# Performance work log

Measured on AMD Instinct MI355X. Metric: run time of the kernel, lower is better.

## Reference

```python
import jax, jax.numpy as jnp
import numpy as np

VOCAB, EMBED, SEQ, UNITS, BATCH = 10000, 100, 80, 64, 16384


def setup_inputs() -> dict:
    key = jax.random.key(0)
    ks = jax.random.split(key, 8)
    s = 0.05
    return {
        "tokens": jax.random.randint(ks[0], (BATCH, SEQ), 0, VOCAB, dtype=jnp.int32),
        "emb": jax.random.normal(ks[1], (VOCAB, EMBED), jnp.float32) * s,
        "Wx1": jax.random.normal(ks[2], (EMBED, UNITS), jnp.float32) * s,
        "Wh1": jax.random.normal(ks[3], (UNITS, UNITS), jnp.float32) * s,
        "b1": jnp.zeros((UNITS,), jnp.float32),
        "Wx2": jax.random.normal(ks[4], (UNITS, UNITS), jnp.float32) * s,
        "Wh2": jax.random.normal(ks[5], (UNITS, UNITS), jnp.float32) * s,
        "b2": jnp.zeros((UNITS,), jnp.float32),
        "Wd": jax.random.normal(ks[6], (UNITS, 1), jnp.float32) * s,
        "bd": jnp.zeros((1,), jnp.float32),
    }


def _simple_rnn(x, Wx, Wh, b):
    """SimpleRNN (eval mode): h_t = tanh(x_t @ Wx + h_{t-1} @ Wh + b).
    x: (B, T, E) -> all hidden states (B, T, U)."""
    # precompute input projection once (big GEMM), scan only does the small recurrent matmul
    xp = jnp.einsum("bte,eu->btu", x, Wx) + b  # (B, T, U)

    def step(h, xt):
        h = jnp.tanh(xt + h @ Wh)
        return h, h

    h0 = jnp.zeros((x.shape[0], Wh.shape[0]), x.dtype)
    _, hs = jax.lax.scan(step, h0, jnp.swapaxes(xp, 0, 1))  # (T, B, U)
    return jnp.swapaxes(hs, 0, 1)  # (B, T, U)


def reference(tokens, emb, Wx1, Wh1, b1, Wx2, Wh2, b2, Wd, bd):
    x = emb[tokens]                              # (B, T, E) embedding lookup
    h1 = _simple_rnn(x, Wx1, Wh1, b1)            # (B, T, U) return_sequences=True
    h2 = _simple_rnn(h1, Wx2, Wh2, b2)[:, -1]    # (B, U)    last state only
    return jax.nn.sigmoid(h2 @ Wd + bd)          # (B, 1)
```

## Files before the change

### kernel.cpp

```cpp
#include <hip/hip_runtime.h>
#include <hip/hip_bf16.h>


#define BATCH 16384
#define SEQ   80
#define EMBED 100
#define UNITS 64
#define ROWS  16
#define VOCAB 10000

typedef __attribute__((ext_vector_type(8))) _Float16 f16x8;
typedef __attribute__((ext_vector_type(4))) float f32x4;
typedef __attribute__((ext_vector_type(2))) float f32x2;
typedef __attribute__((ext_vector_type(4))) int   i32x4;
typedef __attribute__((ext_vector_type(2))) int   i32x2;

using h2 = decltype(__builtin_amdgcn_cvt_pkrtz(0.f, 0.f));

static __device__ __forceinline__ f32x2 tanh2(f32x2 x) {
    f32x2 u = x * x;
    f32x2 w = x * u;
    f32x2 p = u * 0.13333333f + (-0.33333333f);
    return w * p + x;
}

static __device__ __forceinline__ f16x8 ash(i32x4 v) {
    return __builtin_bit_cast(f16x8, v);
}

__global__ __launch_bounds__(256) void xp_prep(const float* __restrict__ emb,
                                               const float* __restrict__ Wx1,
                                               const float* __restrict__ b1,
                                               float* __restrict__ xp) {
    const int v = blockIdx.x * 4 + (threadIdx.x >> 6);
    const int u = threadIdx.x & 63;
    const float* er = emb + (size_t)v * EMBED;
    const float* wc = Wx1 + u;
    float acc = b1[u];
#pragma unroll 5
    for (int k4 = 0; k4 < EMBED / 4; ++k4) {
        f32x4 e = *reinterpret_cast<const f32x4*>(er + k4 * 4);
        acc += e[0] * wc[(k4 * 4 + 0) * UNITS];
        acc += e[1] * wc[(k4 * 4 + 1) * UNITS];
        acc += e[2] * wc[(k4 * 4 + 2) * UNITS];
        acc += e[3] * wc[(k4 * 4 + 3) * UNITS];
    }
    xp[(size_t)v * UNITS + u] = acc;
}

__global__ __launch_bounds__(64)
void rnn_fused(const int* __restrict__ tokens,
               const float* __restrict__ xpT,
               const float* __restrict__ Wh1,
               const float* __restrict__ Wx2,
               const float* __restrict__ Wh2,
               const float* __restrict__ b2,
               const float* __restrict__ Wd,
               const float* __restrict__ bd,
               float* __restrict__ out)
{
    __shared__ int tokL[ROWS][SEQ + 1];

    const int lane = threadIdx.x;
    const int c    = lane & 15;
    const int q    = lane >> 4;
    const int rowBase = blockIdx.x * ROWS;

    for (int i = lane; i < ROWS * SEQ; i += 64) {
        int r = i / SEQ, tt = i - r * SEQ;
        tokL[r][tt] = tokens[rowBase * SEQ + i];
    }
    __syncthreads();

    auto loadW = [&](const float* W, f16x8 (&dst)[2][4]) {
#pragma unroll
        for (int kt = 0; kt < 2; ++kt)
#pragma unroll
            for (int mt = 0; mt < 4; ++mt) {
                f16x8 v;
#pragma unroll
                for (int j = 0; j < 8; ++j) {
                    int u = kt * 32 + ((j >> 2) << 4) + q * 4 + (j & 3);
                    v[j] = (_Float16)W[u * UNITS + mt * 16 + c];
                }
                dst[kt][mt] = v;
            }
    };

    f16x8 awh1[2][4], awx2[2][4], awh2[2][4];
    loadW(Wh1, awh1);
    loadW(Wx2, awx2);
    loadW(Wh2, awh2);

    f32x4 b2C[4];
#pragma unroll
    for (int mt = 0; mt < 4; ++mt)
#pragma unroll
        for (int r = 0; r < 4; ++r)
            b2C[mt][r] = b2[mt * 16 + q * 4 + r];

    const h2 kC1h = __builtin_amdgcn_cvt_pkrtz( 0.13333333f,  0.13333333f);
    const h2 kC0h = __builtin_amdgcn_cvt_pkrtz(-0.33333333f, -0.33333333f);

    auto tanh_pack4 = [&](f32x4 v) -> i32x2 {
        h2 lo = __builtin_amdgcn_cvt_pkrtz(v[0], v[1]);
        h2 hi = __builtin_amdgcn_cvt_pkrtz(v[2], v[3]);
        h2 ulo = lo * lo,        uhi = hi * hi;
        h2 wlo = ulo * lo,       whi = uhi * hi;
        h2 plo = ulo * kC1h + kC0h, phi = uhi * kC1h + kC0h;
        h2 rlo = wlo * plo + lo, rhi = whi * phi + hi;
        i32x2 r;
        r[0] = __builtin_bit_cast(int, rlo);
        r[1] = __builtin_bit_cast(int, rhi);
        return r;
    };

    const int* tokC = &tokL[c][0];

    auto gatherXP = [&](int tk, f32x4 (&dst)[4]) {
        const float* p = xpT + (unsigned)tk * UNITS + q * 4;
        dst[0] = *reinterpret_cast<const f32x4*>(p);
        dst[1] = *reinterpret_cast<const f32x4*>(p + 16);
        dst[2] = *reinterpret_cast<const f32x4*>(p + 32);
        dst[3] = *reinterpret_cast<const f32x4*>(p + 48);
    };

    i32x4 h1[2] = {(i32x4){0,0,0,0}, (i32x4){0,0,0,0}};
    i32x4 h2s[2] = {(i32x4){0,0,0,0}, (i32x4){0,0,0,0}};
    f32x4 xp0[4], xp1[4];
    gatherXP(tokC[0], xp0);
    gatherXP(tokC[1], xp1);

    auto tanhP = [&](f32x4 (&a)[4], i32x4 (&h)[2]) {
        i32x2 p0 = tanh_pack4(a[0]), p1 = tanh_pack4(a[1]);
        i32x2 p2 = tanh_pack4(a[2]), p3 = tanh_pack4(a[3]);
        h[0] = (i32x4){p0[0], p0[1], p1[0], p1[1]};
        h[1] = (i32x4){p2[0], p2[1], p3[0], p3[1]};
    };

    auto body = [&](f32x4 (&xpS)[4], bool doPre, int tp) {
        f32x4 aL1[4], aL2[4];
#pragma unroll
        for (int mt = 0; mt < 4; ++mt)
            aL1[mt] = __builtin_amdgcn_mfma_f32_16x16x32_f16(awh1[0][mt], ash(h1[0]), xpS[mt], 0, 0, 0);
#pragma unroll
        for (int mt = 0; mt < 4; ++mt)
            aL2[mt] = __builtin_amdgcn_mfma_f32_16x16x32_f16(awx2[0][mt], ash(h1[0]), b2C[mt], 0, 0, 0);
#pragma unroll
        for (int mt = 0; mt < 4; ++mt)
            aL1[mt] = __builtin_amdgcn_mfma_f32_16x16x32_f16(awh1[1][mt], ash(h1[1]), aL1[mt], 0, 0, 0);
#pragma unroll
        for (int mt = 0; mt < 4; ++mt)
            aL2[mt] = __builtin_amdgcn_mfma_f32_16x16x32_f16(awx2[1][mt], ash(h1[1]), aL2[mt], 0, 0, 0);
#pragma unroll
        for (int mt = 0; mt < 4; ++mt)
            aL2[mt] = __builtin_amdgcn_mfma_f32_16x16x32_f16(awh2[0][mt], ash(h2s[0]), aL2[mt], 0, 0, 0);
#pragma unroll
        for (int mt = 0; mt < 4; ++mt)
            aL2[mt] = __builtin_amdgcn_mfma_f32_16x16x32_f16(awh2[1][mt], ash(h2s[1]), aL2[mt], 0, 0, 0);
        if (doPre) gatherXP(tp, xpS);
        tanhP(aL1, h1);
        tanhP(aL2, h2s);
    };

    {
        f32x4 aL1[4];
#pragma unroll
        for (int mt = 0; mt < 4; ++mt)
            aL1[mt] = __builtin_amdgcn_mfma_f32_16x16x32_f16(awh1[0][mt], ash(h1[0]), xp0[mt], 0, 0, 0);
#pragma unroll
        for (int mt = 0; mt < 4; ++mt)
            aL1[mt] = __builtin_amdgcn_mfma_f32_16x16x32_f16(awh1[1][mt], ash(h1[1]), aL1[mt], 0, 0, 0);
        gatherXP(tokC[2], xp0);
        tanhP(aL1, h1);
    }

#pragma unroll 1
    for (int tt = 1; tt <= 75; tt += 2) {
        body(xp1, true, tokC[tt + 2]);
        body(xp0, true, tokC[tt + 3]);
    }
    body(xp1, true, tokC[79]);
    body(xp0, false, 0);
    body(xp1, false, 0);

    {
        f32x4 a[4];
#pragma unroll
        for (int mt = 0; mt < 4; ++mt)
            a[mt] = __builtin_amdgcn_mfma_f32_16x16x32_f16(awx2[0][mt], ash(h1[0]), b2C[mt], 0, 0, 0);
#pragma unroll
        for (int mt = 0; mt < 4; ++mt)
            a[mt] = __builtin_amdgcn_mfma_f32_16x16x32_f16(awx2[1][mt], ash(h1[1]), a[mt], 0, 0, 0);
#pragma unroll
        for (int mt = 0; mt < 4; ++mt)
            a[mt] = __builtin_amdgcn_mfma_f32_16x16x32_f16(awh2[0][mt], ash(h2s[0]), a[mt], 0, 0, 0);
#pragma unroll
        for (int mt = 0; mt < 4; ++mt)
            a[mt] = __builtin_amdgcn_mfma_f32_16x16x32_f16(awh2[1][mt], ash(h2s[1]), a[mt], 0, 0, 0);

        f32x4 wdC[4];
#pragma unroll
        for (int mt = 0; mt < 4; ++mt)
#pragma unroll
            for (int r = 0; r < 4; ++r)
                wdC[mt][r] = Wd[mt * 16 + q * 4 + r];
        const float bdv = bd[0];

        float p = 0.f;
#pragma unroll
        for (int mt = 0; mt < 4; ++mt) {
            f32x2 lo = tanh2((f32x2){a[mt][0], a[mt][1]});
            f32x2 hi = tanh2((f32x2){a[mt][2], a[mt][3]});
            p += lo[0] * wdC[mt][0] + lo[1] * wdC[mt][1]
               + hi[0] * wdC[mt][2] + hi[1] * wdC[mt][3];
        }
        p += __shfl_xor(p, 16);
        p += __shfl_xor(p, 32);
        if (q == 0) {
            float x = p + bdv;
            out[rowBase + c] = __builtin_amdgcn_rcpf(1.0f + __expf(-x));
        }
    }
}

extern "C" void kernel_launch(void* const* d_in, const int* in_sizes, int n_in,
                              void* d_out, int out_size, void* d_ws, size_t ws_size,
                              hipStream_t stream) {
    const int*   tokens = (const int*)  d_in[0];
    const float* emb    = (const float*)d_in[1];
    const float* Wx1    = (const float*)d_in[2];
    const float* Wh1    = (const float*)d_in[3];
    const float* b1     = (const float*)d_in[4];
    const float* Wx2    = (const float*)d_in[5];
    const float* Wh2    = (const float*)d_in[6];
    const float* b2     = (const float*)d_in[7];
    const float* Wd     = (const float*)d_in[8];
    const float* bd     = (const float*)d_in[9];
    float* out = (float*)d_out;

    float* xp = (float*)d_ws;
    xp_prep<<<dim3(VOCAB / 4), dim3(256), 0, stream>>>(emb, Wx1, b1, xp);

    dim3 grid(BATCH / ROWS);
    dim3 block(64);
    rnn_fused<<<grid, block, 0, stream>>>(tokens, xp, Wh1, Wx2, Wh2, b2, Wd, bd, out);
}
```

Baseline: 130.5 us.

## Split RNN layers into producer/consumer wavefronts with LDS ring buffer

Runs layer 1 (and the layer-2 input projection) on wave 0 and the layer-2 recurrence on wave 1, passing projected inputs through a 4-slot LDS ring buffer guarded by spin-waited atomic flags. This shortens each wave's serial dependency chain so the two recurrences can overlap instead of running back to back in one wave. It doubles threads per block and adds LDS traffic, spin-wait overhead and occupancy pressure, and it relies on relaxed atomics for memory ordering.

```diff
diff --git a/kernel.cpp b/kernel.cpp
--- a/kernel.cpp
+++ b/kernel.cpp
@@ -15,7 +15,7 @@
 typedef __attribute__((ext_vector_type(4))) int   i32x4;
 typedef __attribute__((ext_vector_type(2))) int   i32x2;
 
-using h2 = decltype(__builtin_amdgcn_cvt_pkrtz(0.f, 0.f));
+using h2t = decltype(__builtin_amdgcn_cvt_pkrtz(0.f, 0.f));
 
 static __device__ __forceinline__ f32x2 tanh2(f32x2 x) {
     f32x2 u = x * x;
@@ -48,7 +48,7 @@
     xp[(size_t)v * UNITS + u] = acc;
 }
 
-__global__ __launch_bounds__(64)
+__global__ __launch_bounds__(128)
 void rnn_fused(const int* __restrict__ tokens,
                const float* __restrict__ xpT,
                const float* __restrict__ Wh1,
@@ -59,18 +59,27 @@
                const float* __restrict__ bd,
                float* __restrict__ out)
 {
-    __shared__ int tokL[ROWS][SEQ + 1];
-
-    const int lane = threadIdx.x;
+    __shared__ int   tokL[ROWS][SEQ + 1];
+    __shared__ float axS[4 * 64 * 16];
+    __shared__ int   prodF, consF;
+
+    const int tid  = threadIdx.x;
+    const int wv   = tid >> 6;
+    const int lane = tid & 63;
     const int c    = lane & 15;
     const int q    = lane >> 4;
     const int rowBase = blockIdx.x * ROWS;
 
-    for (int i = lane; i < ROWS * SEQ; i += 64) {
+    if (tid == 0) { prodF = 0; consF = 0; }
+    for (int i = tid; i < ROWS * SEQ; i += 128) {
         int r = i / SEQ, tt = i - r * SEQ;
         tokL[r][tt] = tokens[rowBase * SEQ + i];
     }
     __syncthreads();
+
+    auto axIdx = [&](int slot, int mt) {
+        return slot * 1024 + lane * 16 + ((mt ^ ((lane >> 1) & 3)) << 2);
+    };
 
     auto loadW = [&](const float* W, f16x8 (&dst)[2][4]) {
 #pragma unroll
@@ -87,50 +96,20 @@
             }
     };
 
-    f16x8 awh1[2][4], awx2[2][4], awh2[2][4];
-    loadW(Wh1, awh1);
-    loadW(Wx2, awx2);
-    loadW(Wh2, awh2);
-
-    f32x4 b2C[4];
-#pragma unroll
-    for (int mt = 0; mt < 4; ++mt)
-#pragma unroll
-        for (int r = 0; r < 4; ++r)
-            b2C[mt][r] = b2[mt * 16 + q * 4 + r];
-
-    const h2 kC1h = __builtin_amdgcn_cvt_pkrtz( 0.13333333f,  0.13333333f);
-    const h2 kC0h = __builtin_amdgcn_cvt_pkrtz(-0.33333333f, -0.33333333f);
-
+    const h2t kC1h = __builtin_amdgcn_cvt_pkrtz( 0.13333333f,  0.13333333f);
+    const h2t kC0h = __builtin_amdgcn_cvt_pkrtz(-0.33333333f, -0.33333333f);
     auto tanh_pack4 = [&](f32x4 v) -> i32x2 {
-        h2 lo = __builtin_amdgcn_cvt_pkrtz(v[0], v[1]);
-        h2 hi = __builtin_amdgcn_cvt_pkrtz(v[2], v[3]);
-        h2 ulo = lo * lo,        uhi = hi * hi;
-        h2 wlo = ulo * lo,       whi = uhi * hi;
-        h2 plo = ulo * kC1h + kC0h, phi = uhi * kC1h + kC0h;
-        h2 rlo = wlo * plo + lo, rhi = whi * phi + hi;
+        h2t lo = __builtin_amdgcn_cvt_pkrtz(v[0], v[1]);
+        h2t hi = __builtin_amdgcn_cvt_pkrtz(v[2], v[3]);
+        h2t ulo = lo * lo,          uhi = hi * hi;
+        h2t wlo = ulo * lo,         whi = uhi * hi;
+        h2t plo = ulo * kC1h + kC0h, phi = uhi * kC1h + kC0h;
+        h2t rlo = wlo * plo + lo,   rhi = whi * phi + hi;
         i32x2 r;
         r[0] = __builtin_bit_cast(int, rlo);
         r[1] = __builtin_bit_cast(int, rhi);
         return r;
     };
-
-    const int* tokC = &tokL[c][0];
-
-    auto gatherXP = [&](int tk, f32x4 (&dst)[4]) {
-        const float* p = xpT + (unsigned)tk * UNITS + q * 4;
-        dst[0] = *reinterpret_cast<const f32x4*>(p);
-        dst[1] = *reinterpret_cast<const f32x4*>(p + 16);
-        dst[2] = *reinterpret_cast<const f32x4*>(p + 32);
-        dst[3] = *reinterpret_cast<const f32x4*>(p + 48);
-    };
-
-    i32x4 h1[2] = {(i32x4){0,0,0,0}, (i32x4){0,0,0,0}};
-    i32x4 h2s[2] = {(i32x4){0,0,0,0}, (i32x4){0,0,0,0}};
-    f32x4 xp0[4], xp1[4];
-    gatherXP(tokC[0], xp0);
-    gatherXP(tokC[1], xp1);
-
     auto tanhP = [&](f32x4 (&a)[4], i32x4 (&h)[2]) {
         i32x2 p0 = tanh_pack4(a[0]), p1 = tanh_pack4(a[1]);
         i32x2 p2 = tanh_pack4(a[2]), p3 = tanh_pack4(a[3]);
@@ -138,67 +117,114 @@
         h[1] = (i32x4){p2[0], p2[1], p3[0], p3[1]};
     };
 
-    auto body = [&](f32x4 (&xpS)[4], bool doPre, int tp) {
-        f32x4 aL1[4], aL2[4];
+    if (wv == 0) {
+        f16x8 awh1[2][4], awx2[2][4];
+        loadW(Wh1, awh1);
+        loadW(Wx2, awx2);
+
+        f32x4 b2C[4];
 #pragma unroll
         for (int mt = 0; mt < 4; ++mt)
-            aL1[mt] = __builtin_amdgcn_mfma_f32_16x16x32_f16(awh1[0][mt], ash(h1[0]), xpS[mt], 0, 0, 0);
-#pragma unroll
-        for (int mt = 0; mt < 4; ++mt)
-            aL2[mt] = __builtin_amdgcn_mfma_f32_16x16x32_f16(awx2[0][mt], ash(h1[0]), b2C[mt], 0, 0, 0);
-#pragma unroll
-        for (int mt = 0; mt < 4; ++mt)
-            aL1[mt] = __builtin_amdgcn_mfma_f32_16x16x32_f16(awh1[1][mt], ash(h1[1]), aL1[mt], 0, 0, 0);
-#pragma unroll
-        for (int mt = 0; mt < 4; ++mt)
-            aL2[mt] = __builtin_amdgcn_mfma_f32_16x16x32_f16(awx2[1][mt], ash(h1[1]), aL2[mt], 0, 0, 0);
-#pragma unroll
-        for (int mt = 0; mt < 4; ++mt)
-            aL2[mt] = __builtin_amdgcn_mfma_f32_16x16x32_f16(awh2[0][mt], ash(h2s[0]), aL2[mt], 0, 0, 0);
-#pragma unroll
-        for (int mt = 0; mt < 4; ++mt)
-            aL2[mt] = __builtin_amdgcn_mfma_f32_16x16x32_f16(awh2[1][mt], ash(h2s[1]), aL2[mt], 0, 0, 0);
-        if (doPre) gatherXP(tp, xpS);
-        tanhP(aL1, h1);
-        tanhP(aL2, h2s);
-    };
-
-    {
-        f32x4 aL1[4];
-#pragma unroll
-        for (int mt = 0; mt < 4; ++mt)
-            aL1[mt] = __builtin_amdgcn_mfma_f32_16x16x32_f16(awh1[0][mt], ash(h1[0]), xp0[mt], 0, 0, 0);
-#pragma unroll
-        for (int mt = 0; mt < 4; ++mt)
-            aL1[mt] = __builtin_amdgcn_mfma_f32_16x16x32_f16(awh1[1][mt], ash(h1[1]), aL1[mt], 0, 0, 0);
-        gatherXP(tokC[2], xp0);
-        tanhP(aL1, h1);
-    }
+#pragma unroll
+            for (int r = 0; r < 4; ++r)
+                b2C[mt][r] = b2[mt * 16 + q * 4 + r];
+
+        const int* tokC = &tokL[c][0];
+        auto gatherXP = [&](int tk, f32x4 (&dst)[4]) {
+            const float* p = xpT + (unsigned)tk * UNITS + q * 4;
+            dst[0] = *reinterpret_cast<const f32x4*>(p);
+            dst[1] = *reinterpret_cast<const f32x4*>(p + 16);
+            dst[2] = *reinterpret_cast<const f32x4*>(p + 32);
+            dst[3] = *reinterpret_cast<const f32x4*>(p + 48);
+        };
+
+        i32x4 h1[2] = {(i32x4){0,0,0,0}, (i32x4){0,0,0,0}};
+        f32x4 xp0[4], xp1[4];
+        gatherXP(tokC[0], xp0);
+        gatherXP(tokC[1], xp1);
+
+        int consNow = 0;
+
+        auto body = [&](int t, f32x4 (&xpS)[4], bool pre, int tp) {
+            consNow = __hip_atomic_load(&consF, __ATOMIC_RELAXED,
+                                        __HIP_MEMORY_SCOPE_WORKGROUP);
+            f32x4 aL1[4], ax[4];
+#pragma unroll
+            for (int mt = 0; mt < 4; ++mt)
+                aL1[mt] = __builtin_amdgcn_mfma_f32_16x16x32_f16(awh1[0][mt], ash(h1[0]), xpS[mt], 0, 0, 0);
+#pragma unroll
+            for (int mt = 0; mt < 4; ++mt)
+                ax[mt] = __builtin_amdgcn_mfma_f32_16x16x32_f16(awx2[0][mt], ash(h1[0]), b2C[mt], 0, 0, 0);
+#pragma unroll
+            for (int mt = 0; mt < 4; ++mt)
+                aL1[mt] = __builtin_amdgcn_mfma_f32_16x16x32_f16(awh1[1][mt], ash(h1[1]), aL1[mt], 0, 0, 0);
+#pragma unroll
+            for (int mt = 0; mt < 4; ++mt)
+                ax[mt] = __builtin_amdgcn_mfma_f32_16x16x32_f16(awx2[1][mt], ash(h1[1]), ax[mt], 0, 0, 0);
+            if (pre) gatherXP(tp, xpS);
+            tanhP(aL1, h1);
+            if (t >= 5) {
+                while (consNow < t - 4) {
+                    __builtin_amdgcn_s_sleep(1);
+                    consNow = __hip_atomic_load(&consF, __ATOMIC_RELAXED,
+                                                __HIP_MEMORY_SCOPE_WORKGROUP);
+                }
+            }
+            const int slot = (t - 1) & 3;
+#pragma unroll
+            for (int mt = 0; mt < 4; ++mt)
+                *reinterpret_cast<f32x4*>(&axS[axIdx(slot, mt)]) = ax[mt];
+            asm volatile("" ::: "memory");
+            __hip_atomic_store(&prodF, t, __ATOMIC_RELAXED,
+                               __HIP_MEMORY_SCOPE_WORKGROUP);
+        };
+
+        {
+            f32x4 aL1[4];
+#pragma unroll
+            for (int mt = 0; mt < 4; ++mt)
+                aL1[mt] = __builtin_amdgcn_mfma_f32_16x16x32_f16(awh1[0][mt], ash(h1[0]), xp0[mt], 0, 0, 0);
+#pragma unroll
+            for (int mt = 0; mt < 4; ++mt)
+                aL1[mt] = __builtin_amdgcn_mfma_f32_16x16x32_f16(awh1[1][mt], ash(h1[1]), aL1[mt], 0, 0, 0);
+            gatherXP(tokC[2], xp0);
+            tanhP(aL1, h1);
+        }
 
 #pragma unroll 1
-    for (int tt = 1; tt <= 75; tt += 2) {
-        body(xp1, true, tokC[tt + 2]);
-        body(xp0, true, tokC[tt + 3]);
-    }
-    body(xp1, true, tokC[79]);
-    body(xp0, false, 0);
-    body(xp1, false, 0);
-
-    {
-        f32x4 a[4];
-#pragma unroll
-        for (int mt = 0; mt < 4; ++mt)
-            a[mt] = __builtin_amdgcn_mfma_f32_16x16x32_f16(awx2[0][mt], ash(h1[0]), b2C[mt], 0, 0, 0);
-#pragma unroll
-        for (int mt = 0; mt < 4; ++mt)
-            a[mt] = __builtin_amdgcn_mfma_f32_16x16x32_f16(awx2[1][mt], ash(h1[1]), a[mt], 0, 0, 0);
-#pragma unroll
-        for (int mt = 0; mt < 4; ++mt)
-            a[mt] = __builtin_amdgcn_mfma_f32_16x16x32_f16(awh2[0][mt], ash(h2s[0]), a[mt], 0, 0, 0);
-#pragma unroll
-        for (int mt = 0; mt < 4; ++mt)
-            a[mt] = __builtin_amdgcn_mfma_f32_16x16x32_f16(awh2[1][mt], ash(h2s[1]), a[mt], 0, 0, 0);
-
+        for (int tt = 1; tt <= 75; tt += 2) {
+            body(tt,     xp1, true, tokC[tt + 2]);
+            body(tt + 1, xp0, true, tokC[tt + 3]);
+        }
+        body(77, xp1, true, tokC[79]);
+        body(78, xp0, false, 0);
+        body(79, xp1, false, 0);
+
+        {
+            while (consNow < 76) {
+                __builtin_amdgcn_s_sleep(1);
+                consNow = __hip_atomic_load(&consF, __ATOMIC_RELAXED,
+                                            __HIP_MEMORY_SCOPE_WORKGROUP);
+            }
+            f32x4 ax[4];
+#pragma unroll
+            for (int mt = 0; mt < 4; ++mt)
+                ax[mt] = __builtin_amdgcn_mfma_f32_16x16x32_f16(awx2[0][mt], ash(h1[0]), b2C[mt], 0, 0, 0);
+#pragma unroll
+            for (int mt = 0; mt < 4; ++mt)
+                ax[mt] = __builtin_amdgcn_mfma_f32_16x16x32_f16(awx2[1][mt], ash(h1[1]), ax[mt], 0, 0, 0);
+            const int slot = 79 & 3;
+#pragma unroll
+            for (int mt = 0; mt < 4; ++mt)
+                *reinterpret_cast<f32x4*>(&axS[axIdx(slot, mt)]) = ax[mt];
+            asm volatile("" ::: "memory");
+            __hip_atomic_store(&prodF, 80, __ATOMIC_RELAXED,
+                               __HIP_MEMORY_SCOPE_WORKGROUP);
+        }
+
+    } else {
+        f16x8 awh2[2][4];
+        loadW(Wh2, awh2);
         f32x4 wdC[4];
 #pragma unroll
         for (int mt = 0; mt < 4; ++mt)
@@ -207,19 +233,47 @@
                 wdC[mt][r] = Wd[mt * 16 + q * 4 + r];
         const float bdv = bd[0];
 
-        float p = 0.f;
-#pragma unroll
-        for (int mt = 0; mt < 4; ++mt) {
-            f32x2 lo = tanh2((f32x2){a[mt][0], a[mt][1]});
-            f32x2 hi = tanh2((f32x2){a[mt][2], a[mt][3]});
-            p += lo[0] * wdC[mt][0] + lo[1] * wdC[mt][1]
-               + hi[0] * wdC[mt][2] + hi[1] * wdC[mt][3];
-        }
-        p += __shfl_xor(p, 16);
-        p += __shfl_xor(p, 32);
-        if (q == 0) {
-            float x = p + bdv;
-            out[rowBase + c] = __builtin_amdgcn_rcpf(1.0f + __expf(-x));
+        i32x4 h2s[2] = {(i32x4){0,0,0,0}, (i32x4){0,0,0,0}};
+
+#pragma unroll 1
+        for (int t = 0; t < SEQ; ++t) {
+            while (__hip_atomic_load(&prodF, __ATOMIC_RELAXED,
+                                     __HIP_MEMORY_SCOPE_WORKGROUP) < t + 1)
+                __builtin_amdgcn_s_sleep(1);
+            asm volatile("" ::: "memory");
+            f32x4 xc[4];
+            const int slot = t & 3;
+#pragma unroll
+            for (int mt = 0; mt < 4; ++mt)
+                xc[mt] = *reinterpret_cast<const f32x4*>(&axS[axIdx(slot, mt)]);
+            asm volatile("s_waitcnt lgkmcnt(0)" ::: "memory");
+            __hip_atomic_store(&consF, t + 1, __ATOMIC_RELAXED,
+                               __HIP_MEMORY_SCOPE_WORKGROUP);
+            f32x4 a2[4];
+#pragma unroll
+            for (int mt = 0; mt < 4; ++mt)
+                a2[mt] = __builtin_amdgcn_mfma_f32_16x16x32_f16(awh2[0][mt], ash(h2s[0]), xc[mt], 0, 0, 0);
+#pragma unroll
+            for (int mt = 0; mt < 4; ++mt)
+                a2[mt] = __builtin_amdgcn_mfma_f32_16x16x32_f16(awh2[1][mt], ash(h2s[1]), a2[mt], 0, 0, 0);
+            if (t < SEQ - 1) {
+                tanhP(a2, h2s);
+            } else {
+                float p = 0.f;
+#pragma unroll
+                for (int mt = 0; mt < 4; ++mt) {
+                    f32x2 lo = tanh2((f32x2){a2[mt][0], a2[mt][1]});
+                    f32x2 hi = tanh2((f32x2){a2[mt][2], a2[mt][3]});
+                    p += lo[0] * wdC[mt][0] + lo[1] * wdC[mt][1]
+                       + hi[0] * wdC[mt][2] + hi[1] * wdC[mt][3];
+                }
+                p += __shfl_xor(p, 16);
+                p += __shfl_xor(p, 32);
+                if (q == 0) {
+                    float x = p + bdv;
+                    out[rowBase + c] = __builtin_amdgcn_rcpf(1.0f + __expf(-x));
+                }
+            }
         }
     }
 }
@@ -243,6 +297,6 @@
     xp_prep<<<dim3(VOCAB / 4), dim3(256), 0, stream>>>(emb, Wx1, b1, xp);
 
     dim3 grid(BATCH / ROWS);
-    dim3 block(64);
+    dim3 block(128);
     rnn_fused<<<grid, block, 0, stream>>>(tokens, xp, Wh1, Wx2, Wh2, b2, Wd, bd, out);
 }
```

Result: slower. 139.8 us (+7.1%).
